# Kernel tuning notes

Hardware: AMD Instinct MI355X
Metric: run time of the kernel (lower is better)

## Reference

```python
import jax, jax.numpy as jnp
import numpy as np

N = 500_000
E = 8_000_000
IN, HID, OUT = 1, 10, 4
BN_EPS = 1e-5


def _lin_init(key, fan_in, fan_out):
    kw, kb = jax.random.split(key)
    s = 1.0 / np.sqrt(fan_in)
    W = jax.random.uniform(kw, (fan_in, fan_out), minval=-s, maxval=s, dtype=jnp.float32)
    b = jax.random.uniform(kb, (fan_out,), minval=-s, maxval=s, dtype=jnp.float32)
    return W, b


def setup_inputs() -> dict:
    key = jax.random.key(0)
    ks = jax.random.split(key, 12)
    x = jax.random.normal(ks[0], (N, IN), dtype=jnp.float32)
    edge_index = jax.random.randint(ks[1], (2, E), 0, N, dtype=jnp.int64)
    edge_attr = jax.random.uniform(ks[2], (E,), dtype=jnp.float32)
    inp = {"x": x, "edge_index": edge_index, "edge_attr": edge_attr}
    dims = [(IN, HID), (HID, HID), (HID, HID)]
    for i, (di, do) in enumerate(dims, start=1):
        k1, k2 = jax.random.split(ks[2 + i])
        W1, b1 = _lin_init(k1, di, do)
        W2, b2 = _lin_init(k2, do, do)
        inp[f"W{i}a"], inp[f"b{i}a"] = W1, b1
        inp[f"W{i}b"], inp[f"b{i}b"] = W2, b2
        inp[f"g{i}"] = jnp.ones((do,), jnp.float32)
        inp[f"be{i}"] = jnp.zeros((do,), jnp.float32)
    Wf, bf = _lin_init(ks[10], 3 * HID, OUT)
    inp["Wf"], inp["bf"] = Wf, bf
    return inp


def _gin_layer(x, src, dst, Wa, ba, Wb, bb, g, be):
    # GINConv (eps=0): h_i = MLP(x_i + sum_{j->i} x_j); Linear->Linear->BatchNorm (train mode)
    agg = jax.ops.segment_sum(x[src], dst, num_segments=N)  # [N, d]
    h = x + agg
    h = h @ Wa + ba
    h = h @ Wb + bb
    mu = jnp.mean(h, axis=0)
    var = jnp.var(h, axis=0)
    return g * (h - mu) * jax.lax.rsqrt(var + BN_EPS) + be


def _modularity(s, src, dst, w):
    two_m = jnp.sum(w)
    pos = jnp.sum(w * jnp.sum(s[src] * s[dst], axis=-1)) / two_m
    deg = jax.ops.segment_sum(w, src, num_segments=N)  # [N]
    ds = (deg @ s) / two_m  # [OUT]
    return pos - jnp.sum(ds * ds)


def reference(x, edge_index, edge_attr,
              W1a, b1a, W1b, b1b, g1, be1,
              W2a, b2a, W2b, b2b, g2, be2,
              W3a, b3a, W3b, b3b, g3, be3,
              Wf, bf):
    src, dst = edge_index[0], edge_index[1]
    x11 = _gin_layer(x, src, dst, W1a, b1a, W1b, b1b, g1, be1)
    x12 = _gin_layer(x11, src, dst, W2a, b2a, W2b, b2b, g2, be2)
    x13 = _gin_layer(x12, src, dst, W3a, b3a, W3b, b3b, g3, be3)
    logits = jnp.concatenate([x11, x12, x13], axis=-1) @ Wf + bf
    s = jax.nn.softmax(logits, axis=-1)
    q = _modularity(s, src, dst, edge_attr)
    return s, q
```

## Files before the change

### kernel.cpp

```cpp
#include <hip/hip_runtime.h>
#include <hip/hip_bf16.h>

#define NN 500000
#define NE 8000000
#define NB 123
#define BSH 12
#define BSZ 4096
#define CAP 69632
#define M 8
#define NAGG (NB * M)
#define BN_EPS 1e-5f

__device__ __forceinline__ float waveReduceF(float v) {
#pragma unroll
    for (int o = 32; o > 0; o >>= 1) v += __shfl_down(v, o, 64);
    return v;
}
__device__ __forceinline__ double waveReduceD(double v) {
#pragma unroll
    for (int o = 32; o > 0; o >>= 1) v += __shfl_down(v, o, 64);
    return v;
}
__device__ __forceinline__ float u2f(unsigned short u) {
    return __bfloat162float(__builtin_bit_cast(__hip_bfloat16, u));
}
__device__ __forceinline__ unsigned short f2u(float f) {
    return __builtin_bit_cast(unsigned short, __float2bfloat16(f));
}

__global__ void initk(int* __restrict__ cur)
{
    if (threadIdx.x < NB) cur[threadIdx.x] = (int)threadIdx.x * CAP;
}

__global__ __launch_bounds__(512) void scatterk(
    const int4* __restrict__ src4, const int4* __restrict__ dst4,
    const float4* __restrict__ w4, int* __restrict__ cur,
    unsigned* __restrict__ pairs, unsigned short* __restrict__ wp)
{
    __shared__ unsigned sEnt[4096];
    __shared__ unsigned short sW[4096];
    __shared__ unsigned char sB[4096];
    __shared__ int h[8][128];
    __shared__ int wOff[8][128];
    __shared__ int bOff[128];
    __shared__ int lb[128];
    __shared__ int tot[128];

    int tid = threadIdx.x, wv = tid >> 6;
    for (int j = tid; j < 8 * 128; j += 512) (&h[0][0])[j] = 0;
    __syncthreads();

    unsigned en[8]; unsigned short wb[8]; int rb[8];
#pragma unroll
    for (int k = 0; k < 2; k++) {
        int q = blockIdx.x * 1024 + k * 512 + tid;
        if (q < NE / 4) {
            int4 s4 = src4[q]; int4 d4 = dst4[q]; float4 ww = w4[q];
            int ss[4] = {s4.x, s4.y, s4.z, s4.w};
            int dd[4] = {d4.x, d4.y, d4.z, d4.w};
            float fw[4] = {ww.x, ww.y, ww.z, ww.w};
#pragma unroll
            for (int i = 0; i < 4; i++) {
                int d = dd[i], b = d >> BSH;
                en[k * 4 + i] = ((unsigned)(d & (BSZ - 1)) << 19) | (unsigned)ss[i];
                wb[k * 4 + i] = f2u(fw[i]);
                int rk = atomicAdd(&h[wv][b], 1);
                rb[k * 4 + i] = (rk << 8) | b;
            }
        } else {
#pragma unroll
            for (int i = 0; i < 4; i++) rb[k * 4 + i] = -1;
        }
    }
    __syncthreads();
    if (tid < NB) {
        int acc = 0;
#pragma unroll
        for (int w = 0; w < 8; w++) { wOff[w][tid] = acc; acc += h[w][tid]; }
        tot[tid] = acc;
        lb[tid] = atomicAdd(&cur[tid], acc);
    }
    __syncthreads();
    if (tid == 0) {
        int acc = 0;
        for (int b = 0; b < NB; b++) { bOff[b] = acc; acc += tot[b]; }
    }
    __syncthreads();
#pragma unroll
    for (int k = 0; k < 8; k++) {
        if (rb[k] >= 0) {
            int b = rb[k] & 255, rk = rb[k] >> 8;
            int pos = bOff[b] + wOff[wv][b] + rk;
            sEnt[pos] = en[k]; sW[pos] = wb[k]; sB[pos] = (unsigned char)b;
        }
    }
    __syncthreads();
    int nE = NE - blockIdx.x * 4096; if (nE > 4096) nE = 4096;
    for (int j = tid; j < nE; j += 512) {
        int b = sB[j];
        int glob = lb[b] + (j - bOff[b]);
        pairs[glob] = sEnt[j];
        wp[glob] = sW[j];
    }
}

__global__ __launch_bounds__(512) void agg1k(
    const unsigned* __restrict__ pairs, const int* __restrict__ cur,
    const float* __restrict__ x, float* __restrict__ slab)
{
    extern __shared__ float t[];
    for (int j = threadIdx.x; j < 2 * BSZ; j += 512) t[j] = 0.f;
    __syncthreads();
    int B = blockIdx.x / M, sl = blockIdx.x % M;
    int b0 = B * CAP;
    int len = cur[B] - b0;
    int seg = (((len + M - 1) / M) + 3) & ~3;
    int lo = b0 + sl * seg;
    int hi = lo + seg, e1 = b0 + len;
    if (hi > e1) hi = e1;
    int n = hi - lo;
    if (n > 0) {
        int nq = n >> 2;
        const uint4* pq = (const uint4*)(pairs + lo);
        for (int i = threadIdx.x; i < nq; i += 512) {
            uint4 p = pq[i];
            float x0 = x[p.x & 524287u];
            float x1 = x[p.y & 524287u];
            float x2 = x[p.z & 524287u];
            float x3 = x[p.w & 524287u];
            atomicAdd(&t[p.x >> 19], x0); atomicAdd(&t[BSZ + (p.x >> 19)], 1.f);
            atomicAdd(&t[p.y >> 19], x1); atomicAdd(&t[BSZ + (p.y >> 19)], 1.f);
            atomicAdd(&t[p.z >> 19], x2); atomicAdd(&t[BSZ + (p.z >> 19)], 1.f);
            atomicAdd(&t[p.w >> 19], x3); atomicAdd(&t[BSZ + (p.w >> 19)], 1.f);
        }
        int rem = n & 3;
        if ((int)threadIdx.x < rem) {
            unsigned p = pairs[lo + (nq << 2) + threadIdx.x];
            atomicAdd(&t[p >> 19], x[p & 524287u]);
            atomicAdd(&t[BSZ + (p >> 19)], 1.f);
        }
    }
    __syncthreads();
    float* sb = slab + (size_t)blockIdx.x * (2 * BSZ);
    for (int j = threadIdx.x; j < 2 * BSZ; j += 512) sb[j] = t[j];
}

__global__ __launch_bounds__(256) void mergeN1(
    const float* __restrict__ slab, const float* __restrict__ x,
    float2* __restrict__ UN2)
{
    int i = blockIdx.x * 256 + threadIdx.x;
    if (i >= NN) return;
    int B = i >> BSH, low = i & (BSZ - 1);
    float sx = 0.f, cn = 0.f;
#pragma unroll
    for (int m = 0; m < M; m++) {
        const float* sb = slab + (size_t)(B * M + m) * (2 * BSZ);
        sx += sb[low];
        cn += sb[BSZ + low];
    }
    UN2[i] = make_float2(x[i] + sx, cn);
}

__global__ __launch_bounds__(512) void agg2k(
    const unsigned* __restrict__ pairs, const int* __restrict__ cur,
    const float2* __restrict__ UN2, float* __restrict__ slab)
{
    extern __shared__ float t[];
    for (int j = threadIdx.x; j < 2 * BSZ; j += 512) t[j] = 0.f;
    __syncthreads();
    int B = blockIdx.x / M, sl = blockIdx.x % M;
    int b0 = B * CAP;
    int len = cur[B] - b0;
    int seg = (((len + M - 1) / M) + 3) & ~3;
    int lo = b0 + sl * seg;
    int hi = lo + seg, e1 = b0 + len;
    if (hi > e1) hi = e1;
    int n = hi - lo;
    if (n > 0) {
        int nq = n >> 2;
        const uint4* pq = (const uint4*)(pairs + lo);
        for (int i = threadIdx.x; i < nq; i += 512) {
            uint4 p = pq[i];
            float2 v0 = UN2[p.x & 524287u];
            float2 v1 = UN2[p.y & 524287u];
            float2 v2 = UN2[p.z & 524287u];
            float2 v3 = UN2[p.w & 524287u];
            atomicAdd(&t[p.x >> 19], v0.x); atomicAdd(&t[BSZ + (p.x >> 19)], v0.y);
            atomicAdd(&t[p.y >> 19], v1.x); atomicAdd(&t[BSZ + (p.y >> 19)], v1.y);
            atomicAdd(&t[p.z >> 19], v2.x); atomicAdd(&t[BSZ + (p.z >> 19)], v2.y);
            atomicAdd(&t[p.w >> 19], v3.x); atomicAdd(&t[BSZ + (p.w >> 19)], v3.y);
        }
        int rem = n & 3;
        if ((int)threadIdx.x < rem) {
            unsigned p = pairs[lo + (nq << 2) + threadIdx.x];
            float2 v = UN2[p & 524287u];
            atomicAdd(&t[p >> 19], v.x);
            atomicAdd(&t[BSZ + (p >> 19)], v.y);
        }
    }
    __syncthreads();
    float* sb = slab + (size_t)blockIdx.x * (2 * BSZ);
    for (int j = threadIdx.x; j < 2 * BSZ; j += 512) sb[j] = t[j];
}

__global__ __launch_bounds__(256) void mergeN2(
    const float* __restrict__ slab, float2* __restrict__ SUN)
{
    int i = blockIdx.x * 256 + threadIdx.x;
    if (i >= NN) return;
    int B = i >> BSH, low = i & (BSZ - 1);
    float su = 0.f, sn = 0.f;
#pragma unroll
    for (int m = 0; m < M; m++) {
        const float* sb = slab + (size_t)(B * M + m) * (2 * BSZ);
        su += sb[low];
        sn += sb[BSZ + low];
    }
    SUN[i] = make_float2(su, sn);
}

__global__ __launch_bounds__(512) void agg3k(
    const unsigned* __restrict__ pairs, const int* __restrict__ cur,
    const float2* __restrict__ SUN, float* __restrict__ slab)
{
    extern __shared__ float t[];
    for (int j = threadIdx.x; j < BSZ; j += 512) t[j] = 0.f;
    __syncthreads();
    int B = blockIdx.x / M, sl = blockIdx.x % M;
    int b0 = B * CAP;
    int len = cur[B] - b0;
    int seg = (((len + M - 1) / M) + 3) & ~3;
    int lo = b0 + sl * seg;
    int hi = lo + seg, e1 = b0 + len;
    if (hi > e1) hi = e1;
    int n = hi - lo;
    if (n > 0) {
        int nq = n >> 2;
        const uint4* pq = (const uint4*)(pairs + lo);
        for (int i = threadIdx.x; i < nq; i += 512) {
            uint4 p = pq[i];
            float v0 = SUN[p.x & 524287u].x;
            float v1 = SUN[p.y & 524287u].x;
            float v2 = SUN[p.z & 524287u].x;
            float v3 = SUN[p.w & 524287u].x;
            atomicAdd(&t[p.x >> 19], v0);
            atomicAdd(&t[p.y >> 19], v1);
            atomicAdd(&t[p.z >> 19], v2);
            atomicAdd(&t[p.w >> 19], v3);
        }
        int rem = n & 3;
        if ((int)threadIdx.x < rem) {
            unsigned p = pairs[lo + (nq << 2) + threadIdx.x];
            atomicAdd(&t[p >> 19], SUN[p & 524287u].x);
        }
    }
    __syncthreads();
    float* sb = slab + (size_t)blockIdx.x * BSZ;
    for (int j = threadIdx.x; j < BSZ; j += 512) sb[j] = t[j];
}

__global__ __launch_bounds__(256) void m3mom(
    const float* __restrict__ slab, const float2* __restrict__ UN2,
    const float2* __restrict__ SUN, float* __restrict__ SSU,
    double* __restrict__ dm)
{
    int i = blockIdx.x * 256 + threadIdx.x;
    double z[5] = {0, 0, 0, 0, 0};
    if (i < NN) {
        int B = i >> BSH, low = i & (BSZ - 1);
        float ssu = 0.f;
#pragma unroll
        for (int m = 0; m < M; m++) ssu += slab[(size_t)(B * M + m) * BSZ + low];
        SSU[i] = ssu;
        float2 un = UN2[i]; float2 ss = SUN[i];
        z[0] = (double)un.x; z[1] = (double)un.y; z[2] = (double)ss.x;
        z[3] = (double)ss.y; z[4] = (double)ssu;
    }
    double m[20];
#pragma unroll
    for (int a = 0; a < 5; a++) m[a] = z[a];
    int idx = 5;
#pragma unroll
    for (int a = 0; a < 5; a++)
#pragma unroll
        for (int b = a; b < 5; b++) m[idx++] = z[a] * z[b];

    __shared__ double part[4][20];
    int lane = threadIdx.x & 63, wid = threadIdx.x >> 6;
#pragma unroll
    for (int k = 0; k < 20; k++) {
        double r = waveReduceD(m[k]);
        if (lane == 0) part[wid][k] = r;
    }
    __syncthreads();
    if (threadIdx.x < 20)
        atomicAdd(&dm[threadIdx.x],
                  part[0][threadIdx.x] + part[1][threadIdx.x] +
                  part[2][threadIdx.x] + part[3][threadIdx.x]);
}

__device__ void mm1010(const float* in, const float* Wa, const float* Wb, float* out)
{
    float t[10];
    for (int m = 0; m < 10; m++) {
        float acc = 0.f;
        for (int k = 0; k < 10; k++) acc += in[k] * Wa[k * 10 + m];
        t[m] = acc;
    }
    for (int j = 0; j < 10; j++) {
        float acc = 0.f;
        for (int m = 0; m < 10; m++) acc += t[m] * Wb[m * 10 + j];
        out[j] = acc;
    }
}

__global__ void constk(
    const float* __restrict__ W1a, const float* __restrict__ b1a,
    const float* __restrict__ W1b, const float* __restrict__ b1b,
    const float* __restrict__ g1, const float* __restrict__ be1,
    const float* __restrict__ W2a, const float* __restrict__ b2a,
    const float* __restrict__ W2b, const float* __restrict__ b2b,
    const float* __restrict__ g2, const float* __restrict__ be2,
    const float* __restrict__ W3a, const float* __restrict__ b3a,
    const float* __restrict__ W3b, const float* __restrict__ b3b,
    const float* __restrict__ g3, const float* __restrict__ be3,
    const float* __restrict__ Wf, const float* __restrict__ bf_,
    const double* __restrict__ dm, float* __restrict__ Lout)
{
    if (threadIdx.x != 0 || blockIdx.x != 0) return;
    const double invN = 1.0 / (double)NN;
    double E[5];
    for (int m = 0; m < 5; m++) E[m] = dm[m] * invN;
    double C[5][5];
    {
        int idx = 5;
        for (int a = 0; a < 5; a++)
            for (int b = a; b < 5; b++) {
                double c = dm[idx++] * invN - E[a] * E[b];
                C[a][b] = c; C[b][a] = c;
            }
    }
    float v[10], c1[10];
    for (int j = 0; j < 10; j++) {
        float av = 0.f, ac = 0.f;
        for (int k = 0; k < 10; k++) {
            av += W1a[k] * W1b[k * 10 + j];
            ac += b1a[k] * W1b[k * 10 + j];
        }
        v[j] = av; c1[j] = ac + b1b[j];
    }
    double Eu = E[0], Vu = C[0][0];
    float p[10], q[10];
    for (int j = 0; j < 10; j++) {
        float var1 = (float)(Vu * (double)v[j] * (double)v[j]);
        float sc1 = g1[j] * rsqrtf(var1 + BN_EPS);
        p[j] = sc1 * v[j];
        q[j] = be1[j] - (float)Eu * p[j];
    }
    float r[10], s[10], d2[10];
    mm1010(p, W2a, W2b, r);
    mm1010(q, W2a, W2b, s);
    for (int j = 0; j < 10; j++) {
        float acc = b2b[j];
        for (int m = 0; m < 10; m++) acc += b2a[m] * W2b[m * 10 + j];
        d2[j] = acc;
    }
    double Ea = E[0] + E[2], Eb = 1.0 + E[1];
    double Va = C[0][0] + 2.0 * C[0][2] + C[2][2];
    double Vb = C[1][1];
    double Cab = C[0][1] + C[2][1];
    float rt[10], st[10], dt[10];
    for (int j = 0; j < 10; j++) {
        double rj = r[j], sj = s[j];
        float var2 = (float)(Va * rj * rj + Vb * sj * sj + 2.0 * Cab * rj * sj);
        float sc2 = g2[j] * rsqrtf(var2 + BN_EPS);
        rt[j] = sc2 * r[j];
        st[j] = sc2 * s[j];
        dt[j] = be2[j] - sc2 * (float)(Ea * rj + Eb * sj);
    }
    float r3[10], s3[10], t3[10], d3[10];
    mm1010(rt, W3a, W3b, r3);
    mm1010(st, W3a, W3b, s3);
    mm1010(dt, W3a, W3b, t3);
    for (int j = 0; j < 10; j++) {
        float acc = b3b[j];
        for (int m = 0; m < 10; m++) acc += b3a[m] * W3b[m * 10 + j];
        d3[j] = acc;
    }
    const double gA[5] = {1, 0, 2, 0, 1};
    const double gB[5] = {0, 2, 0, 1, 0};
    const double gC[5] = {0, 1, 0, 0, 0};
    double EA = E[0] + 2.0 * E[2] + E[4];
    double EB = 1.0 + 2.0 * E[1] + E[3];
    double EC = 1.0 + E[1];
    double VA = 0, VB = 0, VC = 0, CAB = 0, CAC = 0, CBC = 0;
    for (int a = 0; a < 5; a++)
        for (int b = 0; b < 5; b++) {
            double c = C[a][b];
            VA  += gA[a] * gA[b] * c;
            VB  += gB[a] * gB[b] * c;
            VC  += gC[a] * gC[b] * c;
            CAB += gA[a] * gB[b] * c;
            CAC += gA[a] * gC[b] * c;
            CBC += gB[a] * gC[b] * c;
        }
    float rh[10], sh[10], th[10], dh[10];
    for (int j = 0; j < 10; j++) {
        double rj = r3[j], sj = s3[j], tj = t3[j];
        float var3 = (float)(VA * rj * rj + VB * sj * sj + VC * tj * tj
                             + 2.0 * (CAB * rj * sj + CAC * rj * tj + CBC * sj * tj));
        float sc3 = g3[j] * rsqrtf(var3 + BN_EPS);
        rh[j] = sc3 * r3[j];
        sh[j] = sc3 * s3[j];
        th[j] = sc3 * t3[j];
        dh[j] = be3[j] - sc3 * (float)(EA * rj + EB * sj + EC * tj);
    }
    for (int k = 0; k < 4; k++) {
        float Lu = 0, Ln = 0, Lsu = 0, Lsn = 0, Lssu = 0, L0 = bf_[k];
        for (int j = 0; j < 10; j++) {
            float wf1 = Wf[j * 4 + k];
            float wf2 = Wf[(10 + j) * 4 + k];
            float wf3 = Wf[(20 + j) * 4 + k];
            Lu   += p[j] * wf1 + rt[j] * wf2 + rh[j] * wf3;
            Ln   += st[j] * wf2 + (2.f * sh[j] + th[j]) * wf3;
            Lsu  += rt[j] * wf2 + 2.f * rh[j] * wf3;
            Lsn  += sh[j] * wf3;
            Lssu += rh[j] * wf3;
            L0   += q[j] * wf1 + (st[j] + dt[j]) * wf2 + (sh[j] + th[j] + dh[j]) * wf3;
        }
        Lout[0 * 4 + k] = Lu;  Lout[1 * 4 + k] = Ln;   Lout[2 * 4 + k] = Lsu;
        Lout[3 * 4 + k] = Lsn; Lout[4 * 4 + k] = Lssu; Lout[5 * 4 + k] = L0;
    }
}

__global__ __launch_bounds__(256) void finalk(
    const float2* __restrict__ UN2, const float2* __restrict__ SUN,
    const float* __restrict__ SSU, const float* __restrict__ L,
    float4* __restrict__ sout, ushort4* __restrict__ sbf)
{
    __shared__ float sL[24];
    if (threadIdx.x < 24) sL[threadIdx.x] = L[threadIdx.x];
    __syncthreads();
    int i = blockIdx.x * 256 + threadIdx.x;
    if (i >= NN) return;
    float2 un = UN2[i]; float2 ss = SUN[i];
    float u = un.x, n = un.y, su = ss.x, sn = ss.y, ssu = SSU[i];
    float lg[4];
#pragma unroll
    for (int k = 0; k < 4; k++)
        lg[k] = sL[k] * u + sL[4 + k] * n + sL[8 + k] * su
              + sL[12 + k] * sn + sL[16 + k] * ssu + sL[20 + k];
    float mx = fmaxf(fmaxf(lg[0], lg[1]), fmaxf(lg[2], lg[3]));
    float e0 = __expf(lg[0] - mx), e1 = __expf(lg[1] - mx);
    float e2 = __expf(lg[2] - mx), e3 = __expf(lg[3] - mx);
    float inv = 1.f / (e0 + e1 + e2 + e3);
    float s0 = e0 * inv, s1 = e1 * inv, s2 = e2 * inv, s3 = e3 * inv;
    sout[i] = make_float4(s0, s1, s2, s3);
    ushort4 pk; pk.x = f2u(s0); pk.y = f2u(s1); pk.z = f2u(s2); pk.w = f2u(s3);
    sbf[i] = pk;
}

__global__ __launch_bounds__(512) void modk(
    const unsigned* __restrict__ pairs, const unsigned short* __restrict__ wp,
    const int* __restrict__ cur, const ushort4* __restrict__ sbf,
    float* __restrict__ scal)
{
    int B = blockIdx.x / M, sl = blockIdx.x % M;
    int b0 = B * CAP;
    int len = cur[B] - b0;
    int seg = (((len + M - 1) / M) + 3) & ~3;
    int lo = b0 + sl * seg;
    int hi = lo + seg, e1 = b0 + len;
    if (hi > e1) hi = e1;
    int n = hi - lo;
    float acc[6] = {0, 0, 0, 0, 0, 0};
    if (n > 0) {
        int nq = n >> 2;
        const uint4* pq = (const uint4*)(pairs + lo);
        const ushort4* wq = (const ushort4*)(wp + lo);
        for (int i = threadIdx.x; i < nq; i += 512) {
            uint4 p = pq[i];
            ushort4 w4v = wq[i];
            ushort4 ua0 = sbf[p.x & 524287u];
            ushort4 ua1 = sbf[p.y & 524287u];
            ushort4 ua2 = sbf[p.z & 524287u];
            ushort4 ua3 = sbf[p.w & 524287u];
            ushort4 ub0 = sbf[(B << BSH) + (int)(p.x >> 19)];
            ushort4 ub1 = sbf[(B << BSH) + (int)(p.y >> 19)];
            ushort4 ub2 = sbf[(B << BSH) + (int)(p.z >> 19)];
            ushort4 ub3 = sbf[(B << BSH) + (int)(p.w >> 19)];
            unsigned short ws[4] = {w4v.x, w4v.y, w4v.z, w4v.w};
            ushort4 uas[4] = {ua0, ua1, ua2, ua3};
            ushort4 ubs[4] = {ub0, ub1, ub2, ub3};
#pragma unroll
            for (int e = 0; e < 4; e++) {
                float we = u2f(ws[e]);
                float ax = u2f(uas[e].x), ay = u2f(uas[e].y);
                float az = u2f(uas[e].z), aw = u2f(uas[e].w);
                float bx = u2f(ubs[e].x), by = u2f(ubs[e].y);
                float bz = u2f(ubs[e].z), bw = u2f(ubs[e].w);
                acc[0] += we;
                acc[1] += we * (ax * bx + ay * by + az * bz + aw * bw);
                acc[2] += we * ax; acc[3] += we * ay;
                acc[4] += we * az; acc[5] += we * aw;
            }
        }
        int rem = n & 3;
        if ((int)threadIdx.x < rem) {
            int idx = lo + (nq << 2) + threadIdx.x;
            unsigned p = pairs[idx];
            float we = u2f(wp[idx]);
            ushort4 ua = sbf[p & 524287u];
            ushort4 ub = sbf[(B << BSH) + (int)(p >> 19)];
            float ax = u2f(ua.x), ay = u2f(ua.y), az = u2f(ua.z), aw = u2f(ua.w);
            float bx = u2f(ub.x), by = u2f(ub.y), bz = u2f(ub.z), bw = u2f(ub.w);
            acc[0] += we;
            acc[1] += we * (ax * bx + ay * by + az * bz + aw * bw);
            acc[2] += we * ax; acc[3] += we * ay;
            acc[4] += we * az; acc[5] += we * aw;
        }
    }
    __shared__ float part[8][6];
    int lane = threadIdx.x & 63, wid = threadIdx.x >> 6;
#pragma unroll
    for (int k = 0; k < 6; k++) {
        float r = waveReduceF(acc[k]);
        if (lane == 0) part[wid][k] = r;
    }
    __syncthreads();
    if (threadIdx.x < 6) {
        float vsum = 0.f;
#pragma unroll
        for (int wdi = 0; wdi < 8; wdi++) vsum += part[wdi][threadIdx.x];
        int off = (threadIdx.x == 0) ? 128 : (threadIdx.x == 1 ? 129 : 130 + threadIdx.x);
        atomicAdd(&scal[off], vsum);
    }
}

__global__ void qk(const float* __restrict__ scal, float* __restrict__ out)
{
    if (threadIdx.x == 0) {
        float inv = 1.f / scal[128];
        float posv = scal[129] * inv;
        float acc = 0.f;
#pragma unroll
        for (int k = 0; k < 4; k++) {
            float d = scal[132 + k] * inv;
            acc += d * d;
        }
        out[(size_t)NN * 4] = posv - acc;
    }
}

extern "C" void kernel_launch(void* const* d_in, const int* in_sizes, int n_in,
                              void* d_out, int out_size, void* d_ws, size_t ws_size,
                              hipStream_t stream) {
    const float* x  = (const float*)d_in[0];
    const int*  ei  = (const int*)d_in[1];
    const int*  src = ei;
    const int*  dst = ei + NE;
    const float* w   = (const float*)d_in[2];
    const float* W1a = (const float*)d_in[3];  const float* b1a = (const float*)d_in[4];
    const float* W1b = (const float*)d_in[5];  const float* b1b = (const float*)d_in[6];
    const float* g1  = (const float*)d_in[7];  const float* be1 = (const float*)d_in[8];
    const float* W2a = (const float*)d_in[9];  const float* b2a = (const float*)d_in[10];
    const float* W2b = (const float*)d_in[11]; const float* b2b = (const float*)d_in[12];
    const float* g2  = (const float*)d_in[13]; const float* be2 = (const float*)d_in[14];
    const float* W3a = (const float*)d_in[15]; const float* b3a = (const float*)d_in[16];
    const float* W3b = (const float*)d_in[17]; const float* b3b = (const float*)d_in[18];
    const float* g3  = (const float*)d_in[19]; const float* be3 = (const float*)d_in[20];
    const float* Wf  = (const float*)d_in[21]; const float* bfb = (const float*)d_in[22];

    float*  sc   = (float*)d_ws;
    int*    sci  = (int*)d_ws;
    double* dm   = (double*)(sc + 384);
    unsigned* pairs = (unsigned*)(sc + 1024);
    unsigned short* wp = (unsigned short*)(pairs + (size_t)NB * CAP);
    float*  slab = (float*)(wp + (size_t)NB * CAP);
    float2* UN2  = (float2*)(slab + (size_t)NAGG * 2 * BSZ);
    float2* SUN  = UN2 + NN;
    float*  SSU  = (float*)(SUN + NN);
    ushort4* sbf = (ushort4*)(SSU + NN);
    float*  sout = (float*)d_out;

    const int NB_N  = (NN + 255) / 256;
    const int NB_EQ = (NE / 4 + 1023) / 1024;

    hipMemsetAsync(sc, 0, 4096, stream);
    initk<<<1, 128, 0, stream>>>(sci + 832);

    scatterk<<<NB_EQ, 512, 0, stream>>>((const int4*)src, (const int4*)dst,
                                        (const float4*)w, sci + 832, pairs, wp);

    agg1k<<<NAGG, 512, 32768, stream>>>(pairs, sci + 832, x, slab);
    mergeN1<<<NB_N, 256, 0, stream>>>(slab, x, UN2);
    agg2k<<<NAGG, 512, 32768, stream>>>(pairs, sci + 832, UN2, slab);
    mergeN2<<<NB_N, 256, 0, stream>>>(slab, SUN);
    agg3k<<<NAGG, 512, 16384, stream>>>(pairs, sci + 832, SUN, slab);
    m3mom<<<NB_N, 256, 0, stream>>>(slab, UN2, SUN, SSU, dm);

    constk<<<1, 64, 0, stream>>>(W1a, b1a, W1b, b1b, g1, be1,
                                 W2a, b2a, W2b, b2b, g2, be2,
                                 W3a, b3a, W3b, b3b, g3, be3,
                                 Wf, bfb, dm, sc + 160);
    finalk<<<NB_N, 256, 0, stream>>>(UN2, SUN, SSU, sc + 160, (float4*)sout, sbf);
    modk<<<NAGG, 512, 0, stream>>>(pairs, wp, sci + 832, sbf, sc);
    qk<<<1, 64, 0, stream>>>(sc, sout);
}
```

Before: 590.5 us.

## Pack value and count into fixed-point u64 LDS atomics, unroll gathers, cache dst colors

The first two aggregation passes now pack the fixed-point feature sum and the in-degree count into one 64-bit integer. This halves the LDS atomics and the slab traffic, replacing two float atomics per edge with one u64 atomic. Edge loops are manually unrolled two-deep with nontemporal loads to put more gathers in flight. modk stages the destination bucket's bf16 softmax rows in shared memory, and SUN is split into separate SU/SN arrays. The fixed-point encoding adds quantization error and relies on value ranges that do not overflow the packed fields.

```diff
diff --git a/kernel.cpp b/kernel.cpp
--- a/kernel.cpp
+++ b/kernel.cpp
@@ -11,6 +11,10 @@
 #define NAGG (NB * M)
 #define BN_EPS 1e-5f
 
+typedef unsigned uv4 __attribute__((ext_vector_type(4)));
+typedef float fv4 __attribute__((ext_vector_type(4)));
+typedef unsigned long long u64;
+
 __device__ __forceinline__ float waveReduceF(float v) {
 #pragma unroll
     for (int o = 32; o > 0; o >>= 1) v += __shfl_down(v, o, 64);
@@ -26,6 +30,10 @@
 }
 __device__ __forceinline__ unsigned short f2u(float f) {
     return __builtin_bit_cast(unsigned short, __float2bfloat16(f));
+}
+__device__ __forceinline__ u64 pk1(float v) {
+    int iv = (int)rintf(v * 268435456.f);
+    return ((u64)(long long)iv << 20) + 1ull;
 }
 
 __global__ void initk(int* __restrict__ cur)
@@ -107,10 +115,10 @@
 
 __global__ __launch_bounds__(512) void agg1k(
     const unsigned* __restrict__ pairs, const int* __restrict__ cur,
-    const float* __restrict__ x, float* __restrict__ slab)
-{
-    extern __shared__ float t[];
-    for (int j = threadIdx.x; j < 2 * BSZ; j += 512) t[j] = 0.f;
+    const float* __restrict__ x, u64* __restrict__ slab)
+{
+    __shared__ u64 t[BSZ];
+    for (int j = threadIdx.x; j < BSZ; j += 512) t[j] = 0ull;
     __syncthreads();
     int B = blockIdx.x / M, sl = blockIdx.x % M;
     int b0 = B * CAP;
@@ -122,53 +130,71 @@
     int n = hi - lo;
     if (n > 0) {
         int nq = n >> 2;
-        const uint4* pq = (const uint4*)(pairs + lo);
-        for (int i = threadIdx.x; i < nq; i += 512) {
-            uint4 p = pq[i];
-            float x0 = x[p.x & 524287u];
-            float x1 = x[p.y & 524287u];
-            float x2 = x[p.z & 524287u];
-            float x3 = x[p.w & 524287u];
-            atomicAdd(&t[p.x >> 19], x0); atomicAdd(&t[BSZ + (p.x >> 19)], 1.f);
-            atomicAdd(&t[p.y >> 19], x1); atomicAdd(&t[BSZ + (p.y >> 19)], 1.f);
-            atomicAdd(&t[p.z >> 19], x2); atomicAdd(&t[BSZ + (p.z >> 19)], 1.f);
-            atomicAdd(&t[p.w >> 19], x3); atomicAdd(&t[BSZ + (p.w >> 19)], 1.f);
+        const uv4* pq = (const uv4*)(pairs + lo);
+        for (int i = threadIdx.x; i < nq; i += 1024) {
+            uv4 pA = __builtin_nontemporal_load(pq + i);
+            int iB = i + 512;
+            bool vB = iB < nq;
+            float a0 = x[pA.x & 524287u];
+            float a1 = x[pA.y & 524287u];
+            float a2 = x[pA.z & 524287u];
+            float a3 = x[pA.w & 524287u];
+            float c0, c1, c2, c3; unsigned d4, d5, d6, d7;
+            if (vB) {
+                uv4 pB = __builtin_nontemporal_load(pq + iB);
+                c0 = x[pB.x & 524287u]; d4 = pB.x >> 19;
+                c1 = x[pB.y & 524287u]; d5 = pB.y >> 19;
+                c2 = x[pB.z & 524287u]; d6 = pB.z >> 19;
+                c3 = x[pB.w & 524287u]; d7 = pB.w >> 19;
+            }
+            atomicAdd(&t[pA.x >> 19], pk1(a0));
+            atomicAdd(&t[pA.y >> 19], pk1(a1));
+            atomicAdd(&t[pA.z >> 19], pk1(a2));
+            atomicAdd(&t[pA.w >> 19], pk1(a3));
+            if (vB) {
+                atomicAdd(&t[d4], pk1(c0));
+                atomicAdd(&t[d5], pk1(c1));
+                atomicAdd(&t[d6], pk1(c2));
+                atomicAdd(&t[d7], pk1(c3));
+            }
         }
         int rem = n & 3;
         if ((int)threadIdx.x < rem) {
             unsigned p = pairs[lo + (nq << 2) + threadIdx.x];
-            atomicAdd(&t[p >> 19], x[p & 524287u]);
-            atomicAdd(&t[BSZ + (p >> 19)], 1.f);
-        }
-    }
-    __syncthreads();
-    float* sb = slab + (size_t)blockIdx.x * (2 * BSZ);
-    for (int j = threadIdx.x; j < 2 * BSZ; j += 512) sb[j] = t[j];
+            atomicAdd(&t[p >> 19], pk1(x[p & 524287u]));
+        }
+    }
+    __syncthreads();
+    u64* sb = slab + (size_t)blockIdx.x * BSZ;
+    for (int j = threadIdx.x; j < BSZ; j += 512)
+        __builtin_nontemporal_store(t[j], sb + j);
 }
 
 __global__ __launch_bounds__(256) void mergeN1(
-    const float* __restrict__ slab, const float* __restrict__ x,
-    float2* __restrict__ UN2)
+    const u64* __restrict__ slab, const float* __restrict__ x,
+    float2* __restrict__ UN2, u64* __restrict__ ENC)
 {
     int i = blockIdx.x * 256 + threadIdx.x;
     if (i >= NN) return;
     int B = i >> BSH, low = i & (BSZ - 1);
-    float sx = 0.f, cn = 0.f;
-#pragma unroll
-    for (int m = 0; m < M; m++) {
-        const float* sb = slab + (size_t)(B * M + m) * (2 * BSZ);
-        sx += sb[low];
-        cn += sb[BSZ + low];
-    }
-    UN2[i] = make_float2(x[i] + sx, cn);
+    u64 s = 0ull;
+#pragma unroll
+    for (int m = 0; m < M; m++)
+        s += __builtin_nontemporal_load(slab + (size_t)(B * M + m) * BSZ + low);
+    unsigned cn = (unsigned)(s & 0xFFFFFull);
+    long long sv = (long long)(s - (u64)cn) >> 20;
+    float u = x[i] + (float)((double)sv * 3.725290298461914e-09);
+    UN2[i] = make_float2(u, (float)cn);
+    long long iu = (long long)rintf(u * 67108864.f);
+    ENC[i] = ((u64)iu << 22) + (u64)cn;
 }
 
 __global__ __launch_bounds__(512) void agg2k(
     const unsigned* __restrict__ pairs, const int* __restrict__ cur,
-    const float2* __restrict__ UN2, float* __restrict__ slab)
-{
-    extern __shared__ float t[];
-    for (int j = threadIdx.x; j < 2 * BSZ; j += 512) t[j] = 0.f;
+    const u64* __restrict__ ENC, u64* __restrict__ slab)
+{
+    __shared__ u64 t[BSZ];
+    for (int j = threadIdx.x; j < BSZ; j += 512) t[j] = 0ull;
     __syncthreads();
     int B = blockIdx.x / M, sl = blockIdx.x % M;
     int b0 = B * CAP;
@@ -180,52 +206,68 @@
     int n = hi - lo;
     if (n > 0) {
         int nq = n >> 2;
-        const uint4* pq = (const uint4*)(pairs + lo);
-        for (int i = threadIdx.x; i < nq; i += 512) {
-            uint4 p = pq[i];
-            float2 v0 = UN2[p.x & 524287u];
-            float2 v1 = UN2[p.y & 524287u];
-            float2 v2 = UN2[p.z & 524287u];
-            float2 v3 = UN2[p.w & 524287u];
-            atomicAdd(&t[p.x >> 19], v0.x); atomicAdd(&t[BSZ + (p.x >> 19)], v0.y);
-            atomicAdd(&t[p.y >> 19], v1.x); atomicAdd(&t[BSZ + (p.y >> 19)], v1.y);
-            atomicAdd(&t[p.z >> 19], v2.x); atomicAdd(&t[BSZ + (p.z >> 19)], v2.y);
-            atomicAdd(&t[p.w >> 19], v3.x); atomicAdd(&t[BSZ + (p.w >> 19)], v3.y);
+        const uv4* pq = (const uv4*)(pairs + lo);
+        for (int i = threadIdx.x; i < nq; i += 1024) {
+            uv4 pA = __builtin_nontemporal_load(pq + i);
+            int iB = i + 512;
+            bool vB = iB < nq;
+            u64 e0 = ENC[pA.x & 524287u];
+            u64 e1v = ENC[pA.y & 524287u];
+            u64 e2 = ENC[pA.z & 524287u];
+            u64 e3 = ENC[pA.w & 524287u];
+            u64 e4, e5, e6, e7; unsigned d4, d5, d6, d7;
+            if (vB) {
+                uv4 pB = __builtin_nontemporal_load(pq + iB);
+                e4 = ENC[pB.x & 524287u]; d4 = pB.x >> 19;
+                e5 = ENC[pB.y & 524287u]; d5 = pB.y >> 19;
+                e6 = ENC[pB.z & 524287u]; d6 = pB.z >> 19;
+                e7 = ENC[pB.w & 524287u]; d7 = pB.w >> 19;
+            }
+            atomicAdd(&t[pA.x >> 19], e0);
+            atomicAdd(&t[pA.y >> 19], e1v);
+            atomicAdd(&t[pA.z >> 19], e2);
+            atomicAdd(&t[pA.w >> 19], e3);
+            if (vB) {
+                atomicAdd(&t[d4], e4);
+                atomicAdd(&t[d5], e5);
+                atomicAdd(&t[d6], e6);
+                atomicAdd(&t[d7], e7);
+            }
         }
         int rem = n & 3;
         if ((int)threadIdx.x < rem) {
             unsigned p = pairs[lo + (nq << 2) + threadIdx.x];
-            float2 v = UN2[p & 524287u];
-            atomicAdd(&t[p >> 19], v.x);
-            atomicAdd(&t[BSZ + (p >> 19)], v.y);
-        }
-    }
-    __syncthreads();
-    float* sb = slab + (size_t)blockIdx.x * (2 * BSZ);
-    for (int j = threadIdx.x; j < 2 * BSZ; j += 512) sb[j] = t[j];
+            atomicAdd(&t[p >> 19], ENC[p & 524287u]);
+        }
+    }
+    __syncthreads();
+    u64* sb = slab + (size_t)blockIdx.x * BSZ;
+    for (int j = threadIdx.x; j < BSZ; j += 512)
+        __builtin_nontemporal_store(t[j], sb + j);
 }
 
 __global__ __launch_bounds__(256) void mergeN2(
-    const float* __restrict__ slab, float2* __restrict__ SUN)
+    const u64* __restrict__ slab, float* __restrict__ SU, float* __restrict__ SN)
 {
     int i = blockIdx.x * 256 + threadIdx.x;
     if (i >= NN) return;
     int B = i >> BSH, low = i & (BSZ - 1);
-    float su = 0.f, sn = 0.f;
-#pragma unroll
-    for (int m = 0; m < M; m++) {
-        const float* sb = slab + (size_t)(B * M + m) * (2 * BSZ);
-        su += sb[low];
-        sn += sb[BSZ + low];
-    }
-    SUN[i] = make_float2(su, sn);
+    u64 s = 0ull;
+#pragma unroll
+    for (int m = 0; m < M; m++)
+        s += __builtin_nontemporal_load(slab + (size_t)(B * M + m) * BSZ + low);
+    unsigned sn = (unsigned)(s & 0x3FFFFFull);
+    long long sv = (long long)(s - (u64)sn) >> 22;
+    float su = (float)((double)sv * 1.4901161193847656e-08);
+    SU[i] = su;
+    SN[i] = (float)sn;
 }
 
 __global__ __launch_bounds__(512) void agg3k(
     const unsigned* __restrict__ pairs, const int* __restrict__ cur,
-    const float2* __restrict__ SUN, float* __restrict__ slab)
-{
-    extern __shared__ float t[];
+    const float* __restrict__ SU, float* __restrict__ slab)
+{
+    __shared__ float t[BSZ];
     for (int j = threadIdx.x; j < BSZ; j += 512) t[j] = 0.f;
     __syncthreads();
     int B = blockIdx.x / M, sl = blockIdx.x % M;
@@ -238,33 +280,50 @@
     int n = hi - lo;
     if (n > 0) {
         int nq = n >> 2;
-        const uint4* pq = (const uint4*)(pairs + lo);
-        for (int i = threadIdx.x; i < nq; i += 512) {
-            uint4 p = pq[i];
-            float v0 = SUN[p.x & 524287u].x;
-            float v1 = SUN[p.y & 524287u].x;
-            float v2 = SUN[p.z & 524287u].x;
-            float v3 = SUN[p.w & 524287u].x;
-            atomicAdd(&t[p.x >> 19], v0);
-            atomicAdd(&t[p.y >> 19], v1);
-            atomicAdd(&t[p.z >> 19], v2);
-            atomicAdd(&t[p.w >> 19], v3);
+        const uv4* pq = (const uv4*)(pairs + lo);
+        for (int i = threadIdx.x; i < nq; i += 1024) {
+            uv4 pA = __builtin_nontemporal_load(pq + i);
+            int iB = i + 512;
+            bool vB = iB < nq;
+            float a0 = SU[pA.x & 524287u];
+            float a1 = SU[pA.y & 524287u];
+            float a2 = SU[pA.z & 524287u];
+            float a3 = SU[pA.w & 524287u];
+            float c0, c1, c2, c3; unsigned d4, d5, d6, d7;
+            if (vB) {
+                uv4 pB = __builtin_nontemporal_load(pq + iB);
+                c0 = SU[pB.x & 524287u]; d4 = pB.x >> 19;
+                c1 = SU[pB.y & 524287u]; d5 = pB.y >> 19;
+                c2 = SU[pB.z & 524287u]; d6 = pB.z >> 19;
+                c3 = SU[pB.w & 524287u]; d7 = pB.w >> 19;
+            }
+            atomicAdd(&t[pA.x >> 19], a0);
+            atomicAdd(&t[pA.y >> 19], a1);
+            atomicAdd(&t[pA.z >> 19], a2);
+            atomicAdd(&t[pA.w >> 19], a3);
+            if (vB) {
+                atomicAdd(&t[d4], c0);
+                atomicAdd(&t[d5], c1);
+                atomicAdd(&t[d6], c2);
+                atomicAdd(&t[d7], c3);
+            }
         }
         int rem = n & 3;
         if ((int)threadIdx.x < rem) {
             unsigned p = pairs[lo + (nq << 2) + threadIdx.x];
-            atomicAdd(&t[p >> 19], SUN[p & 524287u].x);
+            atomicAdd(&t[p >> 19], SU[p & 524287u]);
         }
     }
     __syncthreads();
     float* sb = slab + (size_t)blockIdx.x * BSZ;
-    for (int j = threadIdx.x; j < BSZ; j += 512) sb[j] = t[j];
+    for (int j = threadIdx.x; j < BSZ; j += 512)
+        __builtin_nontemporal_store(t[j], sb + j);
 }
 
 __global__ __launch_bounds__(256) void m3mom(
     const float* __restrict__ slab, const float2* __restrict__ UN2,
-    const float2* __restrict__ SUN, float* __restrict__ SSU,
-    double* __restrict__ dm)
+    const float* __restrict__ SU, const float* __restrict__ SN,
+    float* __restrict__ SSU, double* __restrict__ dm)
 {
     int i = blockIdx.x * 256 + threadIdx.x;
     double z[5] = {0, 0, 0, 0, 0};
@@ -272,11 +331,12 @@
         int B = i >> BSH, low = i & (BSZ - 1);
         float ssu = 0.f;
 #pragma unroll
-        for (int m = 0; m < M; m++) ssu += slab[(size_t)(B * M + m) * BSZ + low];
+        for (int m = 0; m < M; m++)
+            ssu += __builtin_nontemporal_load(slab + (size_t)(B * M + m) * BSZ + low);
         SSU[i] = ssu;
-        float2 un = UN2[i]; float2 ss = SUN[i];
-        z[0] = (double)un.x; z[1] = (double)un.y; z[2] = (double)ss.x;
-        z[3] = (double)ss.y; z[4] = (double)ssu;
+        float2 un = UN2[i];
+        z[0] = (double)un.x; z[1] = (double)un.y; z[2] = (double)SU[i];
+        z[3] = (double)SN[i]; z[4] = (double)ssu;
     }
     double m[20];
 #pragma unroll
@@ -436,8 +496,9 @@
 }
 
 __global__ __launch_bounds__(256) void finalk(
-    const float2* __restrict__ UN2, const float2* __restrict__ SUN,
-    const float* __restrict__ SSU, const float* __restrict__ L,
+    const float2* __restrict__ UN2, const float* __restrict__ SU,
+    const float* __restrict__ SN, const float* __restrict__ SSU,
+    const float* __restrict__ L,
     float4* __restrict__ sout, ushort4* __restrict__ sbf)
 {
     __shared__ float sL[24];
@@ -445,8 +506,8 @@
     __syncthreads();
     int i = blockIdx.x * 256 + threadIdx.x;
     if (i >= NN) return;
-    float2 un = UN2[i]; float2 ss = SUN[i];
-    float u = un.x, n = un.y, su = ss.x, sn = ss.y, ssu = SSU[i];
+    float2 un = UN2[i];
+    float u = un.x, n = un.y, su = SU[i], sn = SN[i], ssu = SSU[i];
     float lg[4];
 #pragma unroll
     for (int k = 0; k < 4; k++)
@@ -457,17 +518,35 @@
     float e2 = __expf(lg[2] - mx), e3 = __expf(lg[3] - mx);
     float inv = 1.f / (e0 + e1 + e2 + e3);
     float s0 = e0 * inv, s1 = e1 * inv, s2 = e2 * inv, s3 = e3 * inv;
-    sout[i] = make_float4(s0, s1, s2, s3);
+    fv4 o = {s0, s1, s2, s3};
+    __builtin_nontemporal_store(o, (fv4*)sout + i);
     ushort4 pk; pk.x = f2u(s0); pk.y = f2u(s1); pk.z = f2u(s2); pk.w = f2u(s3);
     sbf[i] = pk;
 }
 
+__device__ __forceinline__ void modacc(u64 ua, u64 ub, float we, float* acc) {
+    float ax = u2f((unsigned short)ua),         ay = u2f((unsigned short)(ua >> 16));
+    float az = u2f((unsigned short)(ua >> 32)), aw = u2f((unsigned short)(ua >> 48));
+    float bx = u2f((unsigned short)ub),         by = u2f((unsigned short)(ub >> 16));
+    float bz = u2f((unsigned short)(ub >> 32)), bw = u2f((unsigned short)(ub >> 48));
+    acc[0] += we;
+    acc[1] += we * (ax * bx + ay * by + az * bz + aw * bw);
+    acc[2] += we * ax; acc[3] += we * ay;
+    acc[4] += we * az; acc[5] += we * aw;
+}
+
 __global__ __launch_bounds__(512) void modk(
     const unsigned* __restrict__ pairs, const unsigned short* __restrict__ wp,
-    const int* __restrict__ cur, const ushort4* __restrict__ sbf,
+    const int* __restrict__ cur, const u64* __restrict__ sbfU,
     float* __restrict__ scal)
 {
+    __shared__ u64 sS[BSZ];
     int B = blockIdx.x / M, sl = blockIdx.x % M;
+    for (int j = threadIdx.x; j < BSZ; j += 512) {
+        int g = (B << BSH) + j;
+        sS[j] = (g < NN) ? sbfU[g] : 0ull;
+    }
+    __syncthreads();
     int b0 = B * CAP;
     int len = cur[B] - b0;
     int seg = (((len + M - 1) / M) + 3) & ~3;
@@ -478,48 +557,42 @@
     float acc[6] = {0, 0, 0, 0, 0, 0};
     if (n > 0) {
         int nq = n >> 2;
-        const uint4* pq = (const uint4*)(pairs + lo);
-        const ushort4* wq = (const ushort4*)(wp + lo);
-        for (int i = threadIdx.x; i < nq; i += 512) {
-            uint4 p = pq[i];
-            ushort4 w4v = wq[i];
-            ushort4 ua0 = sbf[p.x & 524287u];
-            ushort4 ua1 = sbf[p.y & 524287u];
-            ushort4 ua2 = sbf[p.z & 524287u];
-            ushort4 ua3 = sbf[p.w & 524287u];
-            ushort4 ub0 = sbf[(B << BSH) + (int)(p.x >> 19)];
-            ushort4 ub1 = sbf[(B << BSH) + (int)(p.y >> 19)];
-            ushort4 ub2 = sbf[(B << BSH) + (int)(p.z >> 19)];
-            ushort4 ub3 = sbf[(B << BSH) + (int)(p.w >> 19)];
-            unsigned short ws[4] = {w4v.x, w4v.y, w4v.z, w4v.w};
-            ushort4 uas[4] = {ua0, ua1, ua2, ua3};
-            ushort4 ubs[4] = {ub0, ub1, ub2, ub3};
-#pragma unroll
-            for (int e = 0; e < 4; e++) {
-                float we = u2f(ws[e]);
-                float ax = u2f(uas[e].x), ay = u2f(uas[e].y);
-                float az = u2f(uas[e].z), aw = u2f(uas[e].w);
-                float bx = u2f(ubs[e].x), by = u2f(ubs[e].y);
-                float bz = u2f(ubs[e].z), bw = u2f(ubs[e].w);
-                acc[0] += we;
-                acc[1] += we * (ax * bx + ay * by + az * bz + aw * bw);
-                acc[2] += we * ax; acc[3] += we * ay;
-                acc[4] += we * az; acc[5] += we * aw;
+        const uv4* pq = (const uv4*)(pairs + lo);
+        const u64* wq = (const u64*)(wp + lo);
+        for (int i = threadIdx.x; i < nq; i += 1024) {
+            uv4 pA = __builtin_nontemporal_load(pq + i);
+            u64 wA = __builtin_nontemporal_load(wq + i);
+            int iB = i + 512;
+            bool vB = iB < nq;
+            u64 a0 = sbfU[pA.x & 524287u];
+            u64 a1 = sbfU[pA.y & 524287u];
+            u64 a2 = sbfU[pA.z & 524287u];
+            u64 a3 = sbfU[pA.w & 524287u];
+            uv4 pB; u64 wB; u64 a4, a5, a6, a7;
+            if (vB) {
+                pB = __builtin_nontemporal_load(pq + iB);
+                wB = __builtin_nontemporal_load(wq + iB);
+                a4 = sbfU[pB.x & 524287u];
+                a5 = sbfU[pB.y & 524287u];
+                a6 = sbfU[pB.z & 524287u];
+                a7 = sbfU[pB.w & 524287u];
+            }
+            modacc(a0, sS[pA.x >> 19], u2f((unsigned short)wA),         acc);
+            modacc(a1, sS[pA.y >> 19], u2f((unsigned short)(wA >> 16)), acc);
+            modacc(a2, sS[pA.z >> 19], u2f((unsigned short)(wA >> 32)), acc);
+            modacc(a3, sS[pA.w >> 19], u2f((unsigned short)(wA >> 48)), acc);
+            if (vB) {
+                modacc(a4, sS[pB.x >> 19], u2f((unsigned short)wB),         acc);
+                modacc(a5, sS[pB.y >> 19], u2f((unsigned short)(wB >> 16)), acc);
+                modacc(a6, sS[pB.z >> 19], u2f((unsigned short)(wB >> 32)), acc);
+                modacc(a7, sS[pB.w >> 19], u2f((unsigned short)(wB >> 48)), acc);
             }
         }
         int rem = n & 3;
         if ((int)threadIdx.x < rem) {
             int idx = lo + (nq << 2) + threadIdx.x;
             unsigned p = pairs[idx];
-            float we = u2f(wp[idx]);
-            ushort4 ua = sbf[p & 524287u];
-            ushort4 ub = sbf[(B << BSH) + (int)(p >> 19)];
-            float ax = u2f(ua.x), ay = u2f(ua.y), az = u2f(ua.z), aw = u2f(ua.w);
-            float bx = u2f(ub.x), by = u2f(ub.y), bz = u2f(ub.z), bw = u2f(ub.w);
-            acc[0] += we;
-            acc[1] += we * (ax * bx + ay * by + az * bz + aw * bw);
-            acc[2] += we * ax; acc[3] += we * ay;
-            acc[4] += we * az; acc[5] += we * aw;
+            modacc(sbfU[p & 524287u], sS[p >> 19], u2f(wp[idx]), acc);
         }
     }
     __shared__ float part[8][6];
@@ -579,10 +652,13 @@
     unsigned* pairs = (unsigned*)(sc + 1024);
     unsigned short* wp = (unsigned short*)(pairs + (size_t)NB * CAP);
     float*  slab = (float*)(wp + (size_t)NB * CAP);
+    u64*    slabU = (u64*)slab;
     float2* UN2  = (float2*)(slab + (size_t)NAGG * 2 * BSZ);
-    float2* SUN  = UN2 + NN;
-    float*  SSU  = (float*)(SUN + NN);
+    float*  SU   = (float*)(UN2 + NN);
+    float*  SN   = SU + NN;
+    float*  SSU  = SN + NN;
     ushort4* sbf = (ushort4*)(SSU + NN);
+    u64*    ENC  = (u64*)(sbf + NN);
     float*  sout = (float*)d_out;
 
     const int NB_N  = (NN + 255) / 256;
@@ -594,18 +670,18 @@
     scatterk<<<NB_EQ, 512, 0, stream>>>((const int4*)src, (const int4*)dst,
                                         (const float4*)w, sci + 832, pairs, wp);
 
-    agg1k<<<NAGG, 512, 32768, stream>>>(pairs, sci + 832, x, slab);
-    mergeN1<<<NB_N, 256, 0, stream>>>(slab, x, UN2);
-    agg2k<<<NAGG, 512, 32768, stream>>>(pairs, sci + 832, UN2, slab);
-    mergeN2<<<NB_N, 256, 0, stream>>>(slab, SUN);
-    agg3k<<<NAGG, 512, 16384, stream>>>(pairs, sci + 832, SUN, slab);
-    m3mom<<<NB_N, 256, 0, stream>>>(slab, UN2, SUN, SSU, dm);
+    agg1k<<<NAGG, 512, 0, stream>>>(pairs, sci + 832, x, slabU);
+    mergeN1<<<NB_N, 256, 0, stream>>>(slabU, x, UN2, ENC);
+    agg2k<<<NAGG, 512, 0, stream>>>(pairs, sci + 832, ENC, slabU);
+    mergeN2<<<NB_N, 256, 0, stream>>>(slabU, SU, SN);
+    agg3k<<<NAGG, 512, 0, stream>>>(pairs, sci + 832, SU, slab);
+    m3mom<<<NB_N, 256, 0, stream>>>(slab, UN2, SU, SN, SSU, dm);
 
     constk<<<1, 64, 0, stream>>>(W1a, b1a, W1b, b1b, g1, be1,
                                  W2a, b2a, W2b, b2b, g2, be2,
                                  W3a, b3a, W3b, b3b, g3, be3,
                                  Wf, bfb, dm, sc + 160);
-    finalk<<<NB_N, 256, 0, stream>>>(UN2, SUN, SSU, sc + 160, (float4*)sout, sbf);
-    modk<<<NAGG, 512, 0, stream>>>(pairs, wp, sci + 832, sbf, sc);
+    finalk<<<NB_N, 256, 0, stream>>>(UN2, SU, SN, SSU, sc + 160, (float4*)sout, sbf);
+    modk<<<NAGG, 512, 0, stream>>>(pairs, wp, sci + 832, (const u64*)sbf, sc);
     qk<<<1, 64, 0, stream>>>(sc, sout);
 }
```

Result: faster. 496.6 us (-15.9%).
